# Performance work log

Measured on AMD Instinct MI355X. Metric: run time of the kernel, lower is better.

Reference implementation:

```python
import jax, jax.numpy as jnp
import numpy as np

N_NODES = 8192
N_EDGES = 131072
EMB_NF = 256
IN_NODE_NF = 64
IN_EDGE_NF = 16


def setup_inputs() -> dict:
    key = jax.random.key(0)
    ks = jax.random.split(key, 8)
    node_emb = jax.random.normal(ks[0], (N_NODES, EMB_NF), dtype=jnp.float32)
    edge_emb = jax.random.normal(ks[1], (N_EDGES, EMB_NF), dtype=jnp.float32)
    # Linear head params (torch nn.Linear: y = x @ W.T + b)
    s = 1.0 / np.sqrt(EMB_NF)
    node_w = jax.random.uniform(ks[2], (IN_NODE_NF, EMB_NF), jnp.float32, -s, s)
    node_b = jax.random.uniform(ks[3], (IN_NODE_NF,), jnp.float32, -s, s)
    edge_w = jax.random.uniform(ks[4], (IN_EDGE_NF, EMB_NF), jnp.float32, -s, s)
    edge_b = jax.random.uniform(ks[5], (IN_EDGE_NF,), jnp.float32, -s, s)
    W = 0.5 * jnp.ones((1,), dtype=jnp.float32)
    b = 0.8 * jnp.ones((1,), dtype=jnp.float32)
    return {"node_emb": node_emb, "edge_emb": edge_emb,
            "node_w": node_w, "node_b": node_b,
            "edge_w": edge_w, "edge_b": edge_b,
            "W": W, "b": b}


def reference(node_emb, edge_emb, node_w, node_b, edge_w, edge_b, W, b):
    # Two linear decode heads
    recon_node_fs = node_emb @ node_w.T + node_b          # [N, in_node_nf]
    recon_edge_fs = edge_emb @ edge_w.T + edge_b          # [E, in_edge_nf]
    # Pairwise squared L2 distance: sum_d (x_i - x_j)^2 = |x_i|^2 + |x_j|^2 - 2 x_i.x_j
    sq = jnp.sum(node_emb * node_emb, axis=1)             # [N]
    d2 = sq[:, None] + sq[None, :] - 2.0 * (node_emb @ node_emb.T)  # [N, N]
    adj_pred = jax.nn.sigmoid(W[0] * d2 + b[0])           # [N, N]
    n = node_emb.shape[0]
    adj_pred = adj_pred * (1.0 - jnp.eye(n, dtype=adj_pred.dtype))  # remove self loops
    return (recon_node_fs, recon_edge_fs, adj_pred)
```

## Files before the change

### kernel.cpp

```cpp
#include <hip/hip_runtime.h>
#include <cstdint>
#include <cstddef>

#define NN 8192
#define NE 131072
#define EMB 256

typedef float f32x4 __attribute__((ext_vector_type(4)));
typedef __bf16 bf16x8 __attribute__((ext_vector_type(8)));

__device__ __forceinline__ unsigned short f2bf(float f) {
  unsigned u = __float_as_uint(f);
  u += 0x7fffu + ((u >> 16) & 1u);
  return (unsigned short)(u >> 16);
}

__device__ __forceinline__ void gload_lds16(const void* g, void* l) {
  __builtin_amdgcn_global_load_lds(
      (const __attribute__((address_space(1))) unsigned int*)g,
      (__attribute__((address_space(3))) unsigned int*)l, 16, 0, 0);
}

__global__ __launch_bounds__(256) void node_prep_kernel(const float* __restrict__ X,
                                                        const float* __restrict__ w,
                                                        const float* __restrict__ bias,
                                                        float* __restrict__ out,
                                                        unsigned short* __restrict__ Xb,
                                                        float* __restrict__ sq) {
  __shared__ float xs[16 * 260];
  int tid = threadIdx.x;
  int n0  = blockIdx.x * 16;
  int r   = tid >> 4, g = tid & 15;

  float s = 0.f;
  #pragma unroll
  for (int kc = 0; kc < 4; ++kc) {
    float4 v = *(const float4*)(X + (size_t)(n0 + r) * EMB + kc * 64 + g * 4);
    *(float4*)(&xs[r * 260 + kc * 64 + g * 4]) = v;
    s += v.x * v.x + v.y * v.y + v.z * v.z + v.w * v.w;
    ushort4 b;
    b.x = f2bf(v.x); b.y = f2bf(v.y); b.z = f2bf(v.z); b.w = f2bf(v.w);
    *(ushort4*)(Xb + (size_t)(n0 + r) * EMB + kc * 64 + g * 4) = b;
  }
  s += __shfl_xor(s, 1); s += __shfl_xor(s, 2);
  s += __shfl_xor(s, 4); s += __shfl_xor(s, 8);
  if (g == 0) sq[n0 + r] = s;
  __syncthreads();

  int o0 = g * 4;
  float acc[4] = {0.f, 0.f, 0.f, 0.f};
  #pragma unroll 4
  for (int k = 0; k < 256; k += 4) {
    float4 x = *(const float4*)(&xs[r * 260 + k]);
    #pragma unroll
    for (int oo = 0; oo < 4; ++oo) {
      float4 wv = *(const float4*)(w + (size_t)(o0 + oo) * EMB + k);
      acc[oo] = fmaf(x.x, wv.x, fmaf(x.y, wv.y, fmaf(x.z, wv.z, fmaf(x.w, wv.w, acc[oo]))));
    }
  }
  float4 o;
  o.x = acc[0] + bias[o0 + 0];
  o.y = acc[1] + bias[o0 + 1];
  o.z = acc[2] + bias[o0 + 2];
  o.w = acc[3] + bias[o0 + 3];
  *(float4*)(out + (size_t)(n0 + r) * 64 + o0) = o;
}

__global__ __launch_bounds__(256) void mega_kernel(const unsigned short* __restrict__ Xb,
                                                   const float* __restrict__ sq,
                                                   const float* __restrict__ Wp,
                                                   const float* __restrict__ bp,
                                                   float* __restrict__ adj_out,
                                                   const float* __restrict__ Xe,
                                                   const float* __restrict__ ew,
                                                   const float* __restrict__ eb,
                                                   float* __restrict__ edge_out) {
  __shared__ __align__(16) char smem[32768];
  int tid = threadIdx.x;
  int b   = blockIdx.x;
  int g   = b / 9, rem = b - g * 9;

  if (rem == 8) {
    float* lds = (float*)smem;
    int e0 = g * 256;
    int lr = tid >> 2, lc = (tid & 3) * 4;

    float4 v[4];
    #pragma unroll
    for (int q = 0; q < 4; ++q)
      v[q] = *(const float4*)(Xe + (size_t)(e0 + lr + q * 64) * EMB + lc);

    float acc[16];
    #pragma unroll
    for (int o = 0; o < 16; ++o) acc[o] = 0.f;

    for (int kc = 0; kc < 16; ++kc) {
      __syncthreads();
      #pragma unroll
      for (int q = 0; q < 4; ++q) {
        float* d = &lds[(lr + q * 64) * 17 + lc];
        d[0] = v[q].x; d[1] = v[q].y; d[2] = v[q].z; d[3] = v[q].w;
      }
      __syncthreads();
      if (kc < 15) {
        #pragma unroll
        for (int q = 0; q < 4; ++q)
          v[q] = *(const float4*)(Xe + (size_t)(e0 + lr + q * 64) * EMB + (kc + 1) * 16 + lc);
      }
      const float* wk0 = ew + kc * 16;
      #pragma unroll
      for (int k = 0; k < 16; ++k) {
        float x = lds[tid * 17 + k];
        #pragma unroll
        for (int o = 0; o < 16; ++o)
          acc[o] = fmaf(x, wk0[(size_t)o * EMB + k], acc[o]);
      }
    }
    #pragma unroll
    for (int o = 0; o < 16; ++o) acc[o] += eb[o];
    float4* dst = (float4*)(edge_out + (size_t)(e0 + tid) * 16);
    dst[0] = make_float4(acc[0], acc[1], acc[2], acc[3]);
    dst[1] = make_float4(acc[4], acc[5], acc[6], acc[7]);
    dst[2] = make_float4(acc[8], acc[9], acc[10], acc[11]);
    dst[3] = make_float4(acc[12], acc[13], acc[14], acc[15]);
    return;
  }

  unsigned short* As = (unsigned short*)smem;
  unsigned short* Bs = As + 128 * 64;

  int adjid = g * 8 + rem;
  int low3  = adjid & 7, q = adjid >> 3;
  int ti = low3 * 8 + (q & 7);
  int tj = ((q >> 6) & 7) * 8 + ((q >> 3) & 7);

  int wave = tid >> 6, lane = tid & 63;
  int wr = (wave >> 1) * 64;
  int wc = (wave & 1) * 64;
  int l15 = lane & 15, lg = lane >> 4;

  f32x4 acc[4][4] = {};

  int r_base = tid >> 3;
  int cb     = (tid & 7) << 4;

  for (int kt = 0; kt < 4; ++kt) {
    #pragma unroll
    for (int it = 0; it < 4; ++it) {
      int r   = it * 32 + r_base;
      int cbs = cb ^ ((r & 7) << 4);
      int col = (kt << 6) + (cbs >> 1);
      const unsigned short* ga = Xb + (size_t)(ti * 128 + r) * EMB + col;
      const unsigned short* gb = Xb + (size_t)(tj * 128 + r) * EMB + col;
      gload_lds16(ga, (char*)As + it * 4096 + wave * 1024);
      gload_lds16(gb, (char*)Bs + it * 4096 + wave * 1024);
    }
    __syncthreads();
    #pragma unroll
    for (int ks = 0; ks < 2; ++ks) {
      bf16x8 af[4], bfr[4];
      #pragma unroll
      for (int m = 0; m < 4; ++m) {
        int rr = wr + m * 16 + l15;
        int bc = ((ks << 6) + (lg << 4)) ^ ((rr & 7) << 4);
        af[m] = *(const bf16x8*)((const char*)As + rr * 128 + bc);
      }
      #pragma unroll
      for (int n = 0; n < 4; ++n) {
        int rr = wc + n * 16 + l15;
        int bc = ((ks << 6) + (lg << 4)) ^ ((rr & 7) << 4);
        bfr[n] = *(const bf16x8*)((const char*)Bs + rr * 128 + bc);
      }
      #pragma unroll
      for (int m = 0; m < 4; ++m)
        #pragma unroll
        for (int n = 0; n < 4; ++n)
          acc[m][n] = __builtin_amdgcn_mfma_f32_16x16x32_bf16(af[m], bfr[n], acc[m][n], 0, 0, 0);
    }
    __syncthreads();
  }

  float W0 = Wp[0], b0 = bp[0];
  float w2 = -2.0f * W0;
  int col0 = tj * 128 + wc + l15;
  int row0 = ti * 128 + wr + (lg << 2);
  bool diag = (ti == tj);

  float aiW[16];
  #pragma unroll
  for (int m = 0; m < 4; ++m)
    #pragma unroll
    for (int rg = 0; rg < 4; ++rg)
      aiW[m * 4 + rg] = W0 * sq[row0 + m * 16 + rg];

  #pragma unroll
  for (int n = 0; n < 4; ++n) {
    int j = col0 + n * 16;
    float sjW = fmaf(W0, sq[j], b0);
    #pragma unroll
    for (int m = 0; m < 4; ++m) {
      #pragma unroll
      for (int rg = 0; rg < 4; ++rg) {
        float t = fmaf(w2, acc[m][n][rg], aiW[m * 4 + rg] + sjW);
        acc[m][n][rg] = __builtin_amdgcn_rcpf(1.0f + __expf(-t));
      }
      if (diag) {
        #pragma unroll
        for (int rg = 0; rg < 4; ++rg)
          if (row0 + m * 16 + rg == j) acc[m][n][rg] = 0.0f;
      }
      __builtin_nontemporal_store(acc[m][n],
          (f32x4*)(&adj_out[(size_t)j * NN + row0 + m * 16]));
    }
  }
}

extern "C" void kernel_launch(void* const* d_in, const int* in_sizes, int n_in,
                              void* d_out, int out_size, void* d_ws, size_t ws_size,
                              hipStream_t stream) {
  const float* node_emb = (const float*)d_in[0];
  const float* edge_emb = (const float*)d_in[1];
  const float* node_w   = (const float*)d_in[2];
  const float* node_b   = (const float*)d_in[3];
  const float* edge_w   = (const float*)d_in[4];
  const float* edge_b   = (const float*)d_in[5];
  const float* Wp       = (const float*)d_in[6];
  const float* bp       = (const float*)d_in[7];

  float* out      = (float*)d_out;
  float* node_out = out;
  float* edge_out = out + (size_t)NN * 64;
  float* adj_out  = out + (size_t)NN * 64 + (size_t)NE * 16;

  unsigned short* Xb = (unsigned short*)d_ws;
  float* sq = (float*)((char*)d_ws + (size_t)NN * EMB * 2);

  node_prep_kernel<<<dim3(512), dim3(256), 0, stream>>>(node_emb, node_w, node_b,
                                                        node_out, Xb, sq);
  mega_kernel<<<dim3(4608), dim3(256), 0, stream>>>(Xb, sq, Wp, bp, adj_out,
                                                    edge_emb, edge_w, edge_b, edge_out);
}
```

Measured before the change: 180.6 us.

## Enlarge adjacency tiles to 256x256 with 512-thread blocks and remap edge blocks

The adjacency GEMM tile grows from 128x128 to 256x256, computed by 8 waves each holding an 8x4 MFMA accumulator grid, with doubled LDS. Edge-head blocks now process 512 edges each and are interleaved among adjacency blocks through a new modular block-ID mapping. The aim is to cut redundant global/L2 loads of Xb per output element and to reduce the number of blocks. In exchange, register pressure and LDS use rise (64KB, launch bounds 512,2), which may reduce occupancy, and the block-to-tile mapping gets more complex.

```diff
diff --git a/kernel.cpp b/kernel.cpp
--- a/kernel.cpp
+++ b/kernel.cpp
@@ -66,29 +66,32 @@
   *(float4*)(out + (size_t)(n0 + r) * 64 + o0) = o;
 }
 
-__global__ __launch_bounds__(256) void mega_kernel(const unsigned short* __restrict__ Xb,
-                                                   const float* __restrict__ sq,
-                                                   const float* __restrict__ Wp,
-                                                   const float* __restrict__ bp,
-                                                   float* __restrict__ adj_out,
-                                                   const float* __restrict__ Xe,
-                                                   const float* __restrict__ ew,
-                                                   const float* __restrict__ eb,
-                                                   float* __restrict__ edge_out) {
-  __shared__ __align__(16) char smem[32768];
+__global__ __launch_bounds__(512, 2) void mega_kernel(const unsigned short* __restrict__ Xb,
+                                                      const float* __restrict__ sq,
+                                                      const float* __restrict__ Wp,
+                                                      const float* __restrict__ bp,
+                                                      float* __restrict__ adj_out,
+                                                      const float* __restrict__ Xe,
+                                                      const float* __restrict__ ew,
+                                                      const float* __restrict__ eb,
+                                                      float* __restrict__ edge_out) {
+  __shared__ __align__(16) char smem[65536];
   int tid = threadIdx.x;
   int b   = blockIdx.x;
-  int g   = b / 9, rem = b - g * 9;
-
-  if (rem == 8) {
-    float* lds = (float*)smem;
-    int e0 = g * 256;
+  int x   = b & 7;
+  int s   = b / 40;
+  int k   = (b % 40) >> 3;
+
+  if (((x + 3 * k) % 5) == 4) {
+    float* xs = (float*)smem;
+    int ebid = x * 32 + s;
+    int e0 = ebid * 512;
     int lr = tid >> 2, lc = (tid & 3) * 4;
 
     float4 v[4];
     #pragma unroll
     for (int q = 0; q < 4; ++q)
-      v[q] = *(const float4*)(Xe + (size_t)(e0 + lr + q * 64) * EMB + lc);
+      v[q] = *(const float4*)(Xe + (size_t)(e0 + lr + q * 128) * EMB + lc);
 
     float acc[16];
     #pragma unroll
@@ -98,22 +101,22 @@
       __syncthreads();
       #pragma unroll
       for (int q = 0; q < 4; ++q) {
-        float* d = &lds[(lr + q * 64) * 17 + lc];
+        float* d = &xs[(lr + q * 128) * 17 + lc];
         d[0] = v[q].x; d[1] = v[q].y; d[2] = v[q].z; d[3] = v[q].w;
       }
       __syncthreads();
       if (kc < 15) {
         #pragma unroll
         for (int q = 0; q < 4; ++q)
-          v[q] = *(const float4*)(Xe + (size_t)(e0 + lr + q * 64) * EMB + (kc + 1) * 16 + lc);
+          v[q] = *(const float4*)(Xe + (size_t)(e0 + lr + q * 128) * EMB + (kc + 1) * 16 + lc);
       }
       const float* wk0 = ew + kc * 16;
       #pragma unroll
-      for (int k = 0; k < 16; ++k) {
-        float x = lds[tid * 17 + k];
+      for (int kk = 0; kk < 16; ++kk) {
+        float xv = xs[tid * 17 + kk];
         #pragma unroll
         for (int o = 0; o < 16; ++o)
-          acc[o] = fmaf(x, wk0[(size_t)o * EMB + k], acc[o]);
+          acc[o] = fmaf(xv, wk0[(size_t)o * EMB + kk], acc[o]);
       }
     }
     #pragma unroll
@@ -127,19 +130,22 @@
   }
 
   unsigned short* As = (unsigned short*)smem;
-  unsigned short* Bs = As + 128 * 64;
-
-  int adjid = g * 8 + rem;
-  int low3  = adjid & 7, q = adjid >> 3;
-  int ti = low3 * 8 + (q & 7);
-  int tj = ((q >> 6) & 7) * 8 + ((q >> 3) & 7);
+  unsigned short* Bs = As + 256 * 64;
+
+  int o = 0;
+  #pragma unroll
+  for (int kk = 0; kk < 4; ++kk)
+    if (kk < k && ((x + 3 * kk) % 5) != 4) ++o;
+  int iloc = 4 * s + o;
+  int ti = x * 4 + (iloc & 3);
+  int tj = iloc >> 2;
 
   int wave = tid >> 6, lane = tid & 63;
-  int wr = (wave >> 1) * 64;
-  int wc = (wave & 1) * 64;
+  int wm = wave >> 2;
+  int wn = wave & 3;
   int l15 = lane & 15, lg = lane >> 4;
 
-  f32x4 acc[4][4] = {};
+  f32x4 acc[8][4] = {};
 
   int r_base = tid >> 3;
   int cb     = (tid & 7) << 4;
@@ -147,32 +153,32 @@
   for (int kt = 0; kt < 4; ++kt) {
     #pragma unroll
     for (int it = 0; it < 4; ++it) {
-      int r   = it * 32 + r_base;
+      int r   = it * 64 + r_base;
       int cbs = cb ^ ((r & 7) << 4);
       int col = (kt << 6) + (cbs >> 1);
-      const unsigned short* ga = Xb + (size_t)(ti * 128 + r) * EMB + col;
-      const unsigned short* gb = Xb + (size_t)(tj * 128 + r) * EMB + col;
-      gload_lds16(ga, (char*)As + it * 4096 + wave * 1024);
-      gload_lds16(gb, (char*)Bs + it * 4096 + wave * 1024);
+      gload_lds16(Xb + (size_t)(ti * 256 + r) * EMB + col,
+                  (char*)As + it * 8192 + wave * 1024);
+      gload_lds16(Xb + (size_t)(tj * 256 + r) * EMB + col,
+                  (char*)Bs + it * 8192 + wave * 1024);
     }
     __syncthreads();
     #pragma unroll
     for (int ks = 0; ks < 2; ++ks) {
-      bf16x8 af[4], bfr[4];
-      #pragma unroll
-      for (int m = 0; m < 4; ++m) {
-        int rr = wr + m * 16 + l15;
+      bf16x8 af[8], bfr[4];
+      #pragma unroll
+      for (int m = 0; m < 8; ++m) {
+        int rr = wm * 128 + m * 16 + l15;
         int bc = ((ks << 6) + (lg << 4)) ^ ((rr & 7) << 4);
         af[m] = *(const bf16x8*)((const char*)As + rr * 128 + bc);
       }
       #pragma unroll
       for (int n = 0; n < 4; ++n) {
-        int rr = wc + n * 16 + l15;
+        int rr = wn * 64 + n * 16 + l15;
         int bc = ((ks << 6) + (lg << 4)) ^ ((rr & 7) << 4);
         bfr[n] = *(const bf16x8*)((const char*)Bs + rr * 128 + bc);
       }
       #pragma unroll
-      for (int m = 0; m < 4; ++m)
+      for (int m = 0; m < 8; ++m)
         #pragma unroll
         for (int n = 0; n < 4; ++n)
           acc[m][n] = __builtin_amdgcn_mfma_f32_16x16x32_bf16(af[m], bfr[n], acc[m][n], 0, 0, 0);
@@ -182,13 +188,13 @@
 
   float W0 = Wp[0], b0 = bp[0];
   float w2 = -2.0f * W0;
-  int col0 = tj * 128 + wc + l15;
-  int row0 = ti * 128 + wr + (lg << 2);
+  int row0 = ti * 256 + wm * 128 + (lg << 2);
+  int col0 = tj * 256 + wn * 64 + l15;
   bool diag = (ti == tj);
 
-  float aiW[16];
-  #pragma unroll
-  for (int m = 0; m < 4; ++m)
+  float aiW[32];
+  #pragma unroll
+  for (int m = 0; m < 8; ++m)
     #pragma unroll
     for (int rg = 0; rg < 4; ++rg)
       aiW[m * 4 + rg] = W0 * sq[row0 + m * 16 + rg];
@@ -198,7 +204,7 @@
     int j = col0 + n * 16;
     float sjW = fmaf(W0, sq[j], b0);
     #pragma unroll
-    for (int m = 0; m < 4; ++m) {
+    for (int m = 0; m < 8; ++m) {
       #pragma unroll
       for (int rg = 0; rg < 4; ++rg) {
         float t = fmaf(w2, acc[m][n][rg], aiW[m * 4 + rg] + sjW);
@@ -237,6 +243,6 @@
 
   node_prep_kernel<<<dim3(512), dim3(256), 0, stream>>>(node_emb, node_w, node_b,
                                                         node_out, Xb, sq);
-  mega_kernel<<<dim3(4608), dim3(256), 0, stream>>>(Xb, sq, Wp, bp, adj_out,
+  mega_kernel<<<dim3(1280), dim3(512), 0, stream>>>(Xb, sq, Wp, bp, adj_out,
                                                     edge_emb, edge_w, edge_b, edge_out);
 }
```

Measured after the change: 194.5 us. 1.08x slower.

## Double-buffer GEMM K-tiles in LDS with 32-wide stages and prefetch

Applied to the files above, without the earlier changes.

Replaces the single-buffered loop of four 64-wide K-tiles with eight 32-wide K-tiles that alternate between two LDS buffers. Each step issues the next tile's global-to-LDS loads before running the current tile's MFMAs, with one barrier per iteration instead of two. The aim is to hide global load latency behind the matrix math. LDS use stays at 32KB, but tiles are smaller, there are twice as many barriers overall, and the XOR swizzle changes to a 4-way pattern that may cause more bank conflicts.

```diff
diff --git a/kernel.cpp b/kernel.cpp
--- a/kernel.cpp
+++ b/kernel.cpp
@@ -126,9 +126,6 @@
     return;
   }
 
-  unsigned short* As = (unsigned short*)smem;
-  unsigned short* Bs = As + 128 * 64;
-
   int adjid = g * 8 + rem;
   int low3  = adjid & 7, q = adjid >> 3;
   int ti = low3 * 8 + (q & 7);
@@ -141,44 +138,51 @@
 
   f32x4 acc[4][4] = {};
 
-  int r_base = tid >> 3;
-  int cb     = (tid & 7) << 4;
-
-  for (int kt = 0; kt < 4; ++kt) {
-    #pragma unroll
-    for (int it = 0; it < 4; ++it) {
-      int r   = it * 32 + r_base;
-      int cbs = cb ^ ((r & 7) << 4);
-      int col = (kt << 6) + (cbs >> 1);
-      const unsigned short* ga = Xb + (size_t)(ti * 128 + r) * EMB + col;
-      const unsigned short* gb = Xb + (size_t)(tj * 128 + r) * EMB + col;
-      gload_lds16(ga, (char*)As + it * 4096 + wave * 1024);
-      gload_lds16(gb, (char*)Bs + it * 4096 + wave * 1024);
-    }
+  int srow0 = wave * 32 + (lane >> 2);
+  int sp    = lane & 3;
+
+  const size_t rowA = (size_t)(ti * 128) * EMB;
+  const size_t rowB = (size_t)(tj * 128) * EMB;
+
+#define STAGE(BUF, KT)                                                          \
+  {                                                                             \
+    char* base = smem + (BUF) * 16384;                                          \
+    int r0 = srow0, r1 = srow0 + 16;                                            \
+    int c0 = (KT) * 32 + ((sp ^ (r0 & 3)) << 3);                                \
+    int c1 = (KT) * 32 + ((sp ^ (r1 & 3)) << 3);                                \
+    gload_lds16(Xb + rowA + (size_t)r0 * EMB + c0, base + wave * 2048);         \
+    gload_lds16(Xb + rowA + (size_t)r1 * EMB + c1, base + wave * 2048 + 1024);  \
+    gload_lds16(Xb + rowB + (size_t)r0 * EMB + c0, base + 8192 + wave * 2048);  \
+    gload_lds16(Xb + rowB + (size_t)r1 * EMB + c1, base + 8192 + wave * 2048 + 1024); \
+  }
+
+  STAGE(0, 0)
+  __syncthreads();
+
+  #pragma unroll
+  for (int kt = 0; kt < 8; ++kt) {
+    if (kt < 7) STAGE((kt + 1) & 1, kt + 1)
+    const char* Ab = smem + (kt & 1) * 16384;
+    const char* Bb = Ab + 8192;
+    bf16x8 af[4], bfr[4];
+    #pragma unroll
+    for (int m = 0; m < 4; ++m) {
+      int rr = wr + m * 16 + l15;
+      af[m] = *(const bf16x8*)(Ab + rr * 64 + ((lg ^ (rr & 3)) << 4));
+    }
+    #pragma unroll
+    for (int n = 0; n < 4; ++n) {
+      int rr = wc + n * 16 + l15;
+      bfr[n] = *(const bf16x8*)(Bb + rr * 64 + ((lg ^ (rr & 3)) << 4));
+    }
+    #pragma unroll
+    for (int m = 0; m < 4; ++m)
+      #pragma unroll
+      for (int n = 0; n < 4; ++n)
+        acc[m][n] = __builtin_amdgcn_mfma_f32_16x16x32_bf16(af[m], bfr[n], acc[m][n], 0, 0, 0);
     __syncthreads();
-    #pragma unroll
-    for (int ks = 0; ks < 2; ++ks) {
-      bf16x8 af[4], bfr[4];
-      #pragma unroll
-      for (int m = 0; m < 4; ++m) {
-        int rr = wr + m * 16 + l15;
-        int bc = ((ks << 6) + (lg << 4)) ^ ((rr & 7) << 4);
-        af[m] = *(const bf16x8*)((const char*)As + rr * 128 + bc);
-      }
-      #pragma unroll
-      for (int n = 0; n < 4; ++n) {
-        int rr = wc + n * 16 + l15;
-        int bc = ((ks << 6) + (lg << 4)) ^ ((rr & 7) << 4);
-        bfr[n] = *(const bf16x8*)((const char*)Bs + rr * 128 + bc);
-      }
-      #pragma unroll
-      for (int m = 0; m < 4; ++m)
-        #pragma unroll
-        for (int n = 0; n < 4; ++n)
-          acc[m][n] = __builtin_amdgcn_mfma_f32_16x16x32_bf16(af[m], bfr[n], acc[m][n], 0, 0, 0);
-    }
-    __syncthreads();
-  }
+  }
+#undef STAGE
 
   float W0 = Wp[0], b0 = bp[0];
   float w2 = -2.0f * W0;
```

Result: faster. 173.4 us (-4.0%).

## Load MFMA operands directly from global memory into registers, dropping LDS staging

Applied to the files above, without the earlier changes.

The adjacency GEMM tiles no longer stage A and B through shared memory with global_load_lds and barriers. Each wave now loads its bf16x8 fragments straight from global memory (L2/L1 cached) into registers, double-buffered across K steps. This removes the LDS round trip and the __syncthreads stalls. In exchange each block issues redundant global loads, because the two waves sharing a row or column tile each fetch it, and it relies on cache hits. The rows are 512-byte strided, so the loads are less coalesced.

```diff
diff --git a/kernel.cpp b/kernel.cpp
--- a/kernel.cpp
+++ b/kernel.cpp
@@ -13,12 +13,6 @@
   unsigned u = __float_as_uint(f);
   u += 0x7fffu + ((u >> 16) & 1u);
   return (unsigned short)(u >> 16);
-}
-
-__device__ __forceinline__ void gload_lds16(const void* g, void* l) {
-  __builtin_amdgcn_global_load_lds(
-      (const __attribute__((address_space(1))) unsigned int*)g,
-      (__attribute__((address_space(3))) unsigned int*)l, 16, 0, 0);
 }
 
 __global__ __launch_bounds__(256) void node_prep_kernel(const float* __restrict__ X,
@@ -75,13 +69,12 @@
                                                    const float* __restrict__ ew,
                                                    const float* __restrict__ eb,
                                                    float* __restrict__ edge_out) {
-  __shared__ __align__(16) char smem[32768];
+  __shared__ float lds[256 * 17];
   int tid = threadIdx.x;
   int b   = blockIdx.x;
   int g   = b / 9, rem = b - g * 9;
 
   if (rem == 8) {
-    float* lds = (float*)smem;
     int e0 = g * 256;
     int lr = tid >> 2, lc = (tid & 3) * 4;
 
@@ -126,9 +119,6 @@
     return;
   }
 
-  unsigned short* As = (unsigned short*)smem;
-  unsigned short* Bs = As + 128 * 64;
-
   int adjid = g * 8 + rem;
   int low3  = adjid & 7, q = adjid >> 3;
   int ti = low3 * 8 + (q & 7);
@@ -141,43 +131,45 @@
 
   f32x4 acc[4][4] = {};
 
-  int r_base = tid >> 3;
-  int cb     = (tid & 7) << 4;
-
-  for (int kt = 0; kt < 4; ++kt) {
-    #pragma unroll
-    for (int it = 0; it < 4; ++it) {
-      int r   = it * 32 + r_base;
-      int cbs = cb ^ ((r & 7) << 4);
-      int col = (kt << 6) + (cbs >> 1);
-      const unsigned short* ga = Xb + (size_t)(ti * 128 + r) * EMB + col;
-      const unsigned short* gb = Xb + (size_t)(tj * 128 + r) * EMB + col;
-      gload_lds16(ga, (char*)As + it * 4096 + wave * 1024);
-      gload_lds16(gb, (char*)Bs + it * 4096 + wave * 1024);
-    }
-    __syncthreads();
-    #pragma unroll
-    for (int ks = 0; ks < 2; ++ks) {
-      bf16x8 af[4], bfr[4];
+  const char* pa[4];
+  const char* pb[4];
+  #pragma unroll
+  for (int m = 0; m < 4; ++m) {
+    pa[m] = (const char*)(Xb + (size_t)(ti * 128 + wr + m * 16 + l15) * EMB + lg * 8);
+    pb[m] = (const char*)(Xb + (size_t)(tj * 128 + wc + m * 16 + l15) * EMB + lg * 8);
+  }
+
+  bf16x8 ae[4], be[4], ao[4], bo[4];
+  #pragma unroll
+  for (int m = 0; m < 4; ++m) {
+    ae[m] = *(const bf16x8*)(pa[m]);
+    be[m] = *(const bf16x8*)(pb[m]);
+  }
+
+  #pragma unroll
+  for (int kp = 0; kp < 4; ++kp) {
+    #pragma unroll
+    for (int m = 0; m < 4; ++m) {
+      ao[m] = *(const bf16x8*)(pa[m] + (2 * kp + 1) * 64);
+      bo[m] = *(const bf16x8*)(pb[m] + (2 * kp + 1) * 64);
+    }
+    #pragma unroll
+    for (int m = 0; m < 4; ++m)
+      #pragma unroll
+      for (int n = 0; n < 4; ++n)
+        acc[m][n] = __builtin_amdgcn_mfma_f32_16x16x32_bf16(ae[m], be[n], acc[m][n], 0, 0, 0);
+    if (kp < 3) {
       #pragma unroll
       for (int m = 0; m < 4; ++m) {
-        int rr = wr + m * 16 + l15;
-        int bc = ((ks << 6) + (lg << 4)) ^ ((rr & 7) << 4);
-        af[m] = *(const bf16x8*)((const char*)As + rr * 128 + bc);
-      }
-      #pragma unroll
-      for (int n = 0; n < 4; ++n) {
-        int rr = wc + n * 16 + l15;
-        int bc = ((ks << 6) + (lg << 4)) ^ ((rr & 7) << 4);
-        bfr[n] = *(const bf16x8*)((const char*)Bs + rr * 128 + bc);
-      }
-      #pragma unroll
-      for (int m = 0; m < 4; ++m)
-        #pragma unroll
-        for (int n = 0; n < 4; ++n)
-          acc[m][n] = __builtin_amdgcn_mfma_f32_16x16x32_bf16(af[m], bfr[n], acc[m][n], 0, 0, 0);
-    }
-    __syncthreads();
+        ae[m] = *(const bf16x8*)(pa[m] + (2 * kp + 2) * 64);
+        be[m] = *(const bf16x8*)(pb[m] + (2 * kp + 2) * 64);
+      }
+    }
+    #pragma unroll
+    for (int m = 0; m < 4; ++m)
+      #pragma unroll
+      for (int n = 0; n < 4; ++n)
+        acc[m][n] = __builtin_amdgcn_mfma_f32_16x16x32_bf16(ao[m], bo[n], acc[m][n], 0, 0, 0);
   }
 
   float W0 = Wp[0], b0 = bp[0];
```

After: 228.7 us. 26.6% more time.
